# Kernel tuning notes

Hardware: AMD Instinct MI355X
Metric: run time of the kernel (lower is better)

The kernel has to match this reference:

```python
import jax, jax.numpy as jnp
import numpy as np

N_NODES = 50000
N_EDGES = 1600000
NFEAT, NHID, NCLASS = 256, 128, 40
DROPOUT_P = 0.5


def gcn_conv(x, W, b, src, dst, n):
    # PyG GCNConv: h = X W; add self-loops; symmetric norm D^-1/2 (A+I) D^-1/2.
    h = x @ W  # [N, out]
    loop = jnp.arange(n, dtype=src.dtype)
    s = jnp.concatenate([src, loop])  # [E+N]
    d = jnp.concatenate([dst, loop])
    deg = jax.ops.segment_sum(jnp.ones_like(d, dtype=h.dtype), d, num_segments=n)  # in-degree incl. self-loop
    dinv = jax.lax.rsqrt(jnp.maximum(deg, 1.0))
    norm = dinv[s] * dinv[d]  # [E+N]
    msg = h[s] * norm[:, None]  # [E+N, out] gather
    out = jax.ops.segment_sum(msg, d, num_segments=n)  # scatter-add
    return out + b


def setup_inputs() -> dict:
    key = jax.random.key(0)
    k = jax.random.split(key, 7)
    x = jax.random.normal(k[0], (N_NODES, NFEAT), dtype=jnp.float32)
    edge_index = jax.random.randint(k[1], (2, N_EDGES), 0, N_NODES, dtype=jnp.int64)
    W1 = jax.random.normal(k[2], (NFEAT, NHID), dtype=jnp.float32) * (1.0 / np.sqrt(NFEAT))
    b1 = jnp.zeros((NHID,), dtype=jnp.float32)
    W2 = jax.random.normal(k[3], (NHID, NCLASS), dtype=jnp.float32) * (1.0 / np.sqrt(NHID))
    b2 = jnp.zeros((NCLASS,), dtype=jnp.float32)
    keep = jax.random.bernoulli(k[4], 1.0 - DROPOUT_P, (N_NODES, NHID))
    drop_mask = keep.astype(jnp.float32) / (1.0 - DROPOUT_P)  # fixed training-mode dropout mask
    return {"x": x, "edge_index": edge_index, "W1": W1, "b1": b1, "W2": W2, "b2": b2, "drop_mask": drop_mask}


def reference(x, edge_index, W1, b1, W2, b2, drop_mask):
    src, dst = edge_index[0], edge_index[1]
    h = gcn_conv(x, W1, b1, src, dst, N_NODES)
    h = jax.nn.relu(h)
    h = h * drop_mask  # F.dropout(training=True) with fixed mask
    h = gcn_conv(h, W2, b2, src, dst, N_NODES)
    return jax.nn.log_softmax(h, axis=1)
```

## Files before the change

### kernel.cpp

```cpp
#include <hip/hip_runtime.h>
#include <hip/hip_fp16.h>
#include <math.h>

#define N_NODES 50000
#define N_EDGES 1600000
#define NFEAT 256
#define NHID 128
#define NCLASS 40

#define BSHIFT 7
#define NBUCK 391
#define CAP 5120
#define EPB 4096
#define SEGN 4
#define SEGSZ 12800

typedef _Float16 f16x8 __attribute__((ext_vector_type(8)));
typedef float f32x4 __attribute__((ext_vector_type(4)));

__global__ __launch_bounds__(256) void k_binA(const int* __restrict__ src,
                                              const int* __restrict__ dst,
                                              int* __restrict__ gcur,
                                              unsigned int* __restrict__ packed) {
    __shared__ int lhist[NBUCK];
    __shared__ int lbase[NBUCK];
    __shared__ int lcur[NBUCK];
    int t = threadIdx.x;
    for (int i = t; i < NBUCK; i += 256) { lhist[i] = 0; lcur[i] = 0; }
    __syncthreads();
    int e0 = blockIdx.x * EPB;
    int e1 = min(e0 + EPB, N_EDGES);
    for (int e = e0 + t; e < e1; e += 256) {
        int b = dst[e] >> BSHIFT;
        atomicAdd(&lhist[b], 1);
    }
    __syncthreads();
    for (int i = t; i < NBUCK; i += 256)
        lbase[i] = atomicAdd(&gcur[i], lhist[i]);
    __syncthreads();
    for (int e = e0 + t; e < e1; e += 256) {
        int d = dst[e];
        int b = d >> BSHIFT;
        int r = atomicAdd(&lcur[b], 1);
        int pos = lbase[b] + r;
        if (pos < CAP)
            packed[(size_t)b * CAP + pos] =
                ((unsigned int)src[e] << BSHIFT) | (unsigned int)(d & 127);
    }
}

__global__ __launch_bounds__(256) void k_binB(const int* __restrict__ gcur,
                                              const unsigned int* __restrict__ packed,
                                              unsigned short* __restrict__ esrc_seg,
                                              unsigned short* __restrict__ esrc_row,
                                              int* __restrict__ sbeg,
                                              int* __restrict__ scnt,
                                              int* __restrict__ row_beg,
                                              int* __restrict__ row_cnt,
                                              float* __restrict__ dinv) {
    __shared__ unsigned int sp[CAP];
    __shared__ int hist[512];
    __shared__ int scan[512];
    __shared__ int cur[512];
    __shared__ int psum[64];
    int b = blockIdx.x;
    int t = threadIdx.x;
    int cnt = min(gcur[b], CAP);
    for (int i = t; i < 512; i += 256) { hist[i] = 0; cur[i] = 0; }
    __syncthreads();
    const unsigned int* pin = packed + (size_t)b * CAP;
    for (int i = t; i < cnt; i += 256) {
        unsigned int w = pin[i];
        sp[i] = w;
        int srcv = (int)(w >> BSHIFT);
        atomicAdd(&hist[(srcv / SEGSZ) * 128 + (int)(w & 127u)], 1);
    }
    __syncthreads();
    if (t < 64) {
        int s = 0;
        #pragma unroll
        for (int j = 0; j < 8; j++) s += hist[t * 8 + j];
        psum[t] = s;
    }
    __syncthreads();
    if (t == 0) {
        int s = 0;
        for (int j = 0; j < 64; j++) { int v = psum[j]; psum[j] = s; s += v; }
    }
    __syncthreads();
    if (t < 64) {
        int s = psum[t];
        #pragma unroll
        for (int j = 0; j < 8; j++) { scan[t * 8 + j] = s; s += hist[t * 8 + j]; }
    }
    __syncthreads();
    for (int i = t; i < cnt; i += 256) {
        unsigned int w = sp[i];
        int srcv = (int)(w >> BSHIFT);
        int key = (srcv / SEGSZ) * 128 + (int)(w & 127u);
        int r = atomicAdd(&cur[key], 1);
        esrc_seg[(size_t)b * CAP + scan[key] + r] = (unsigned short)srcv;
    }
    if (t < 128) {
        int node = b * 128 + t;
        if (node < N_NODES) {
            int tot = 0;
            #pragma unroll
            for (int s = 0; s < SEGN; s++) {
                sbeg[node * 4 + s] = b * CAP + scan[s * 128 + t];
                scnt[node * 4 + s] = hist[s * 128 + t];
                tot += hist[s * 128 + t];
            }
            row_cnt[node] = tot;
            dinv[node] = rsqrtf((float)(tot + 1));
        }
    }
    __syncthreads();
    if (t < 128) { hist[t] = 0; cur[t] = 0; }
    __syncthreads();
    for (int i = t; i < cnt; i += 256) atomicAdd(&hist[sp[i] & 127u], 1);
    __syncthreads();
    if (t == 0) {
        int s = 0;
        for (int j = 0; j < 128; j++) { int v = hist[j]; scan[j] = s; s += v; }
    }
    __syncthreads();
    for (int i = t; i < cnt; i += 256) {
        unsigned int w = sp[i];
        int dl = (int)(w & 127u);
        int r = atomicAdd(&cur[dl], 1);
        esrc_row[(size_t)b * CAP + scan[dl] + r] = (unsigned short)(w >> BSHIFT);
    }
    if (t < 128) {
        int node = b * 128 + t;
        if (node < N_NODES) row_beg[node] = b * CAP + scan[t];
    }
}

__global__ __launch_bounds__(256) void k_prep(const float* __restrict__ W1,
                                              const float* __restrict__ W2,
                                              __half* __restrict__ w1t,
                                              __half* __restrict__ w2t,
                                              int* __restrict__ gcur) {
    int t = blockIdx.x * 256 + threadIdx.x;
    if (t < NBUCK) gcur[t] = 0;
    if (t < 128 * 256) {
        int n = t >> 8, k = t & 255;
        w1t[t] = __float2half(W1[k * NHID + n]);
    }
    if (t < 48 * 128) {
        int n = t >> 7, k = t & 127;
        w2t[t] = __float2half(n < NCLASS ? W2[k * NCLASS + n] : 0.0f);
    }
}

#define G1_LDA 72
#define G1_LDB 72
#define G1_LDE 136
__global__ __launch_bounds__(256) void k_gemm1(const float* __restrict__ x,
                                               const __half* __restrict__ w1t,
                                               __half* __restrict__ h1h) {
    __shared__ __half smem[64 * G1_LDA + 128 * G1_LDB];
    __half* sA = smem;
    __half* sB = smem + 64 * G1_LDA;
    int t = threadIdx.x;
    int rbase = blockIdx.x * 64;
    int lane = t & 63, wv = t >> 6;
    int m = lane & 15, quad = lane >> 4;
    f32x4 acc[8];
    #pragma unroll
    for (int i = 0; i < 8; i++) acc[i] = (f32x4)0.0f;

    int arow = t >> 2, aseg = t & 3;
    int grow = rbase + arow;
    bool avalid = grow < N_NODES;
    int bn = t >> 1, bseg = t & 1;

    for (int k0 = 0; k0 < NFEAT; k0 += 64) {
        const float4* gs = (const float4*)(x + (size_t)grow * NFEAT + k0 + aseg * 16);
        __half* ad = sA + arow * G1_LDA + aseg * 16;
        #pragma unroll
        for (int i = 0; i < 4; i++) {
            float4 v = avalid ? gs[i] : make_float4(0.f, 0.f, 0.f, 0.f);
            __half2 h0 = __float22half2_rn(make_float2(v.x, v.y));
            __half2 h1 = __float22half2_rn(make_float2(v.z, v.w));
            uint2 st;
            st.x = __builtin_bit_cast(unsigned int, h0);
            st.y = __builtin_bit_cast(unsigned int, h1);
            *(uint2*)(ad + i * 4) = st;
        }
        const uint4* ws4 = (const uint4*)(w1t + bn * NFEAT + k0 + bseg * 32);
        uint4* bd = (uint4*)(sB + bn * G1_LDB + bseg * 32);
        #pragma unroll
        for (int i = 0; i < 4; i++) bd[i] = ws4[i];
        __syncthreads();
        #pragma unroll
        for (int kk = 0; kk < 64; kk += 32) {
            f16x8 af = *(const f16x8*)(sA + (wv * 16 + m) * G1_LDA + kk + quad * 8);
            #pragma unroll
            for (int t8 = 0; t8 < 8; t8++) {
                f16x8 bf = *(const f16x8*)(sB + (t8 * 16 + m) * G1_LDB + kk + quad * 8);
                acc[t8] = __builtin_amdgcn_mfma_f32_16x16x32_f16(af, bf, acc[t8], 0, 0, 0);
            }
        }
        __syncthreads();
    }
    __half* eb = smem;
    #pragma unroll
    for (int t8 = 0; t8 < 8; t8++) {
        #pragma unroll
        for (int r = 0; r < 4; r++)
            eb[(wv * 16 + quad * 4 + r) * G1_LDE + t8 * 16 + m] = __float2half(acc[t8][r]);
    }
    __syncthreads();
    if (avalid) {
        const uint4* es = (const uint4*)(eb + arow * G1_LDE + aseg * 32);
        uint4* od = (uint4*)(h1h + (size_t)grow * NHID + aseg * 32);
        #pragma unroll
        for (int i = 0; i < 4; i++) od[i] = es[i];
    }
}

#define G2_LDA 136
#define G2_LDB 136
#define G2_LDE 72
__global__ __launch_bounds__(256) void k_gemm2(const __half* __restrict__ h1p,
                                               const __half* __restrict__ w2t,
                                               __half* __restrict__ h2p) {
    __shared__ __half smem[64 * G2_LDA + 48 * G2_LDB];
    __half* sA = smem;
    __half* sB = smem + 64 * G2_LDA;
    int t = threadIdx.x;
    int rbase = blockIdx.x * 64;
    int lane = t & 63, wv = t >> 6;
    int m = lane & 15, quad = lane >> 4;
    f32x4 acc[3];
    #pragma unroll
    for (int i = 0; i < 3; i++) acc[i] = (f32x4)0.0f;

    int arow = t >> 2, aseg = t & 3;
    int grow = rbase + arow;
    bool avalid = grow < N_NODES;

    #pragma unroll
    for (int i = 0; i < 3; i++) {
        int idx = t + i * 256;
        int n = idx >> 4, seg = idx & 15;
        *(uint4*)(sB + n * G2_LDB + seg * 8) = *(const uint4*)(w2t + n * NHID + seg * 8);
    }
    {
        const uint4* gs = (const uint4*)(h1p + (size_t)grow * NHID + aseg * 32);
        uint4* ad = (uint4*)(sA + arow * G2_LDA + aseg * 32);
        uint4 z; z.x = z.y = z.z = z.w = 0;
        #pragma unroll
        for (int i = 0; i < 4; i++) ad[i] = avalid ? gs[i] : z;
    }
    __syncthreads();
    #pragma unroll
    for (int kk = 0; kk < 128; kk += 32) {
        f16x8 af = *(const f16x8*)(sA + (wv * 16 + m) * G2_LDA + kk + quad * 8);
        #pragma unroll
        for (int t3 = 0; t3 < 3; t3++) {
            f16x8 bf = *(const f16x8*)(sB + (t3 * 16 + m) * G2_LDB + kk + quad * 8);
            acc[t3] = __builtin_amdgcn_mfma_f32_16x16x32_f16(af, bf, acc[t3], 0, 0, 0);
        }
    }
    __syncthreads();
    __half* eb = smem;
    #pragma unroll
    for (int t3 = 0; t3 < 3; t3++) {
        #pragma unroll
        for (int r = 0; r < 4; r++)
            eb[(wv * 16 + quad * 4 + r) * G2_LDE + t3 * 16 + m] = __float2half(acc[t3][r]);
    }
    {
        int zr = t >> 2, zc = 48 + (t & 3) * 4;
        uint2 z; z.x = z.y = 0;
        *(uint2*)(eb + zr * G2_LDE + zc) = z;
    }
    __syncthreads();
    #pragma unroll
    for (int i = 0; i < 2; i++) {
        int idx = t + i * 256;
        int row = idx >> 3, seg = idx & 7;
        int gr = rbase + row;
        if (gr < N_NODES)
            *(uint4*)(h2p + (size_t)gr * 64 + seg * 8) = *(const uint4*)(eb + row * G2_LDE + seg * 8);
    }
}

__device__ __forceinline__ void acc8f(float* acc, uint4 v, float d) {
    float2 a0 = __half22float2(__builtin_bit_cast(__half2, v.x));
    float2 a1 = __half22float2(__builtin_bit_cast(__half2, v.y));
    float2 a2 = __half22float2(__builtin_bit_cast(__half2, v.z));
    float2 a3 = __half22float2(__builtin_bit_cast(__half2, v.w));
    acc[0] = fmaf(a0.x, d, acc[0]); acc[1] = fmaf(a0.y, d, acc[1]);
    acc[2] = fmaf(a1.x, d, acc[2]); acc[3] = fmaf(a1.y, d, acc[3]);
    acc[4] = fmaf(a2.x, d, acc[4]); acc[5] = fmaf(a2.y, d, acc[5]);
    acc[6] = fmaf(a3.x, d, acc[6]); acc[7] = fmaf(a3.y, d, acc[7]);
}

__global__ __launch_bounds__(256) void k_agg1(const __half* __restrict__ h1h,
                                              const float* __restrict__ dinv,
                                              const int* __restrict__ sbeg,
                                              const int* __restrict__ scnt,
                                              const unsigned short* __restrict__ esrc_seg,
                                              const float* __restrict__ b1,
                                              const float* __restrict__ mask,
                                              __half* __restrict__ h1p) {
    int t = threadIdx.x;
    int qw = t >> 4, ln = t & 15;
    int nbase = blockIdx.x * 64;
    const uint4* hv4 = (const uint4*)h1h;
    __half2 hacc[4][4];
    __half2 hz = __half2half2(__float2half(0.0f));
    #pragma unroll
    for (int k = 0; k < 4; k++) {
        hacc[k][0] = hz; hacc[k][1] = hz; hacc[k][2] = hz; hacc[k][3] = hz;
    }
    for (int s = 0; s < SEGN; s++) {
        #pragma unroll
        for (int k = 0; k < 4; k++) {
            int node = nbase + qw * 4 + k;
            if (node >= N_NODES) continue;
            int beg = sbeg[node * 4 + s];
            int cn = scnt[node * 4 + s];
            for (int e0 = 0; e0 < cn; e0 += 16) {
                int idx = e0 + ln;
                int sv = (idx < cn) ? (int)esrc_seg[beg + idx] : 0;
                float dv = (idx < cn) ? dinv[sv] : 0.0f;
                int n4 = min(16, cn - e0);
                n4 = (n4 + 3) & ~3;
                for (int j = 0; j < n4; j += 4) {
                    int base = qw * 16 + j;
                    int sA = __shfl(sv, base + 0); float dA = __shfl(dv, base + 0);
                    int sB = __shfl(sv, base + 1); float dB = __shfl(dv, base + 1);
                    int sC = __shfl(sv, base + 2); float dC = __shfl(dv, base + 2);
                    int sD = __shfl(sv, base + 3); float dD = __shfl(dv, base + 3);
                    uint4 vA = hv4[(size_t)sA * 16 + ln];
                    uint4 vB = hv4[(size_t)sB * 16 + ln];
                    uint4 vC = hv4[(size_t)sC * 16 + ln];
                    uint4 vD = hv4[(size_t)sD * 16 + ln];
                    __half2 hA = __half2half2(__float2half(dA));
                    __half2 hB = __half2half2(__float2half(dB));
                    __half2 hC = __half2half2(__float2half(dC));
                    __half2 hD = __half2half2(__float2half(dD));
                    hacc[k][0] = __hfma2(__builtin_bit_cast(__half2, vA.x), hA, hacc[k][0]);
                    hacc[k][1] = __hfma2(__builtin_bit_cast(__half2, vA.y), hA, hacc[k][1]);
                    hacc[k][2] = __hfma2(__builtin_bit_cast(__half2, vA.z), hA, hacc[k][2]);
                    hacc[k][3] = __hfma2(__builtin_bit_cast(__half2, vA.w), hA, hacc[k][3]);
                    hacc[k][0] = __hfma2(__builtin_bit_cast(__half2, vB.x), hB, hacc[k][0]);
                    hacc[k][1] = __hfma2(__builtin_bit_cast(__half2, vB.y), hB, hacc[k][1]);
                    hacc[k][2] = __hfma2(__builtin_bit_cast(__half2, vB.z), hB, hacc[k][2]);
                    hacc[k][3] = __hfma2(__builtin_bit_cast(__half2, vB.w), hB, hacc[k][3]);
                    hacc[k][0] = __hfma2(__builtin_bit_cast(__half2, vC.x), hC, hacc[k][0]);
                    hacc[k][1] = __hfma2(__builtin_bit_cast(__half2, vC.y), hC, hacc[k][1]);
                    hacc[k][2] = __hfma2(__builtin_bit_cast(__half2, vC.z), hC, hacc[k][2]);
                    hacc[k][3] = __hfma2(__builtin_bit_cast(__half2, vC.w), hC, hacc[k][3]);
                    hacc[k][0] = __hfma2(__builtin_bit_cast(__half2, vD.x), hD, hacc[k][0]);
                    hacc[k][1] = __hfma2(__builtin_bit_cast(__half2, vD.y), hD, hacc[k][1]);
                    hacc[k][2] = __hfma2(__builtin_bit_cast(__half2, vD.z), hD, hacc[k][2]);
                    hacc[k][3] = __hfma2(__builtin_bit_cast(__half2, vD.w), hD, hacc[k][3]);
                }
            }
        }
    }
    #pragma unroll
    for (int k = 0; k < 4; k++) {
        int node = nbase + qw * 4 + k;
        if (node >= N_NODES) continue;
        float di = dinv[node];
        float acc[8];
        #pragma unroll
        for (int k2 = 0; k2 < 4; k2++) {
            float2 f = __half22float2(hacc[k][k2]);
            acc[2 * k2] = f.x; acc[2 * k2 + 1] = f.y;
        }
        uint4 sv4 = hv4[(size_t)node * 16 + ln];
        acc8f(acc, sv4, di);
        float4 bb0 = ((const float4*)b1)[ln * 2];
        float4 bb1 = ((const float4*)b1)[ln * 2 + 1];
        const float4* mrow = (const float4*)(mask + (size_t)node * NHID);
        float4 mm0 = mrow[ln * 2];
        float4 mm1 = mrow[ln * 2 + 1];
        float o0 = fmaxf(fmaf(acc[0], di, bb0.x), 0.f) * mm0.x;
        float o1 = fmaxf(fmaf(acc[1], di, bb0.y), 0.f) * mm0.y;
        float o2 = fmaxf(fmaf(acc[2], di, bb0.z), 0.f) * mm0.z;
        float o3 = fmaxf(fmaf(acc[3], di, bb0.w), 0.f) * mm0.w;
        float o4 = fmaxf(fmaf(acc[4], di, bb1.x), 0.f) * mm1.x;
        float o5 = fmaxf(fmaf(acc[5], di, bb1.y), 0.f) * mm1.y;
        float o6 = fmaxf(fmaf(acc[6], di, bb1.z), 0.f) * mm1.z;
        float o7 = fmaxf(fmaf(acc[7], di, bb1.w), 0.f) * mm1.w;
        __half2 p0 = __float22half2_rn(make_float2(o0, o1));
        __half2 p1 = __float22half2_rn(make_float2(o2, o3));
        __half2 p2 = __float22half2_rn(make_float2(o4, o5));
        __half2 p3 = __float22half2_rn(make_float2(o6, o7));
        uint4 st;
        st.x = __builtin_bit_cast(unsigned int, p0);
        st.y = __builtin_bit_cast(unsigned int, p1);
        st.z = __builtin_bit_cast(unsigned int, p2);
        st.w = __builtin_bit_cast(unsigned int, p3);
        ((uint4*)h1p)[(size_t)node * 16 + ln] = st;
    }
}

__global__ __launch_bounds__(64) void k_agg2(const __half* __restrict__ h2p,
                                             const float* __restrict__ dinv,
                                             const int* __restrict__ row_beg,
                                             const int* __restrict__ row_cnt,
                                             const unsigned short* __restrict__ esrc,
                                             const float* __restrict__ b2,
                                             float* __restrict__ out) {
    int i = blockIdx.x;
    int lane = threadIdx.x;
    int o8 = lane >> 3;
    int fl = lane & 7;
    const uint4* hv4 = (const uint4*)h2p;
    float di = dinv[i];
    __half2 hacc[4];
    __half2 hz = __half2half2(__float2half(0.0f));
    hacc[0] = hz; hacc[1] = hz; hacc[2] = hz; hacc[3] = hz;
    int s0 = row_beg[i], cnt = row_cnt[i];
    for (int base = 0; base < cnt; base += 64) {
        int idx = base + lane;
        int sv = (idx < cnt) ? (int)esrc[s0 + idx] : 0;
        float dv = (idx < cnt) ? dinv[sv] : 0.0f;
        int n = min(64, cnt - base);
        int nr = (n + 31) & ~31;
        for (int j = 0; j < nr; j += 32) {
            int ss[4]; __half2 dd[4]; uint4 vv[4];
            #pragma unroll
            for (int k = 0; k < 4; k++) {
                int jx = j + 8 * k + o8;
                ss[k] = __shfl(sv, jx);
                float df = __shfl(dv, jx);
                dd[k] = __half2half2(__float2half(df));
            }
            #pragma unroll
            for (int k = 0; k < 4; k++) vv[k] = hv4[(size_t)ss[k] * 8 + fl];
            #pragma unroll
            for (int k = 0; k < 4; k++) {
                hacc[0] = __hfma2(__builtin_bit_cast(__half2, vv[k].x), dd[k], hacc[0]);
                hacc[1] = __hfma2(__builtin_bit_cast(__half2, vv[k].y), dd[k], hacc[1]);
                hacc[2] = __hfma2(__builtin_bit_cast(__half2, vv[k].z), dd[k], hacc[2]);
                hacc[3] = __hfma2(__builtin_bit_cast(__half2, vv[k].w), dd[k], hacc[3]);
            }
        }
    }
    float acc[8];
    #pragma unroll
    for (int k2 = 0; k2 < 4; k2++) {
        float2 f = __half22float2(hacc[k2]);
        acc[2 * k2] = f.x; acc[2 * k2 + 1] = f.y;
    }
    if (o8 == 0) {
        uint4 sv4 = hv4[(size_t)i * 8 + fl];
        acc8f(acc, sv4, di);
    }
    #pragma unroll
    for (int k = 0; k < 8; k++) {
        acc[k] += __shfl_xor(acc[k], 8);
        acc[k] += __shfl_xor(acc[k], 16);
        acc[k] += __shfl_xor(acc[k], 32);
    }
    if (o8 == 0) {
        bool act = (fl < 5);
        float val[8];
        float m = -INFINITY;
        if (act) {
            float4 bb0 = ((const float4*)b2)[fl * 2];
            float4 bb1 = ((const float4*)b2)[fl * 2 + 1];
            val[0] = fmaf(acc[0], di, bb0.x);
            val[1] = fmaf(acc[1], di, bb0.y);
            val[2] = fmaf(acc[2], di, bb0.z);
            val[3] = fmaf(acc[3], di, bb0.w);
            val[4] = fmaf(acc[4], di, bb1.x);
            val[5] = fmaf(acc[5], di, bb1.y);
            val[6] = fmaf(acc[6], di, bb1.z);
            val[7] = fmaf(acc[7], di, bb1.w);
            #pragma unroll
            for (int k = 0; k < 8; k++) m = fmaxf(m, val[k]);
        }
        m = fmaxf(m, __shfl_xor(m, 1));
        m = fmaxf(m, __shfl_xor(m, 2));
        m = fmaxf(m, __shfl_xor(m, 4));
        float ss = 0.f;
        if (act) {
            #pragma unroll
            for (int k = 0; k < 8; k++) ss += expf(val[k] - m);
        }
        ss += __shfl_xor(ss, 1);
        ss += __shfl_xor(ss, 2);
        ss += __shfl_xor(ss, 4);
        if (act) {
            float ls = m + logf(ss);
            float4 r0 = make_float4(val[0] - ls, val[1] - ls, val[2] - ls, val[3] - ls);
            float4 r1 = make_float4(val[4] - ls, val[5] - ls, val[6] - ls, val[7] - ls);
            float4* orow = (float4*)(out + (size_t)i * NCLASS + fl * 8);
            orow[0] = r0;
            orow[1] = r1;
        }
    }
}

extern "C" void kernel_launch(void* const* d_in, const int* in_sizes, int n_in,
                              void* d_out, int out_size, void* d_ws, size_t ws_size,
                              hipStream_t stream) {
    const float* x    = (const float*)d_in[0];
    const int*   ei   = (const int*)d_in[1];
    const float* W1   = (const float*)d_in[2];
    const float* b1   = (const float*)d_in[3];
    const float* W2   = (const float*)d_in[4];
    const float* b2   = (const float*)d_in[5];
    const float* mask = (const float*)d_in[6];
    float* out = (float*)d_out;

    const int* src = ei;
    const int* dst = ei + N_EDGES;

    char* ws = (char*)d_ws;
    size_t off = 0;
    __half* h1p    = (__half*)(ws + off); off += (size_t)N_NODES * NHID * 2;
    __half* h1h    = (__half*)(ws + off); off += (size_t)N_NODES * NHID * 2;
    unsigned short* esrc_seg = (unsigned short*)(ws + off);
    off += ((size_t)NBUCK * CAP * 2 + 255) & ~(size_t)255;
    unsigned short* esrc_row = (unsigned short*)(ws + off);
    off += ((size_t)NBUCK * CAP * 2 + 255) & ~(size_t)255;
    int*   sbeg    = (int*)   (ws + off); off += (size_t)N_NODES * 4 * 4;
    int*   scnt    = (int*)   (ws + off); off += (size_t)N_NODES * 4 * 4;
    float* dinv    = (float*) (ws + off); off += 200192;
    int*   row_beg = (int*)   (ws + off); off += 200192;
    int*   row_cnt = (int*)   (ws + off); off += 200192;
    int*   gcur    = (int*)   (ws + off); off += 4096;
    __half* w1t    = (__half*)(ws + off); off += 128 * 256 * 2;
    __half* w2t    = (__half*)(ws + off); off += 48 * 128 * 2;

    unsigned int* packed = (unsigned int*)h1p;
    __half* h2p = h1h;

    k_prep<<<128, 256, 0, stream>>>(W1, W2, w1t, w2t, gcur);
    k_binA<<<(N_EDGES + EPB - 1) / EPB, 256, 0, stream>>>(src, dst, gcur, packed);
    k_binB<<<NBUCK, 256, 0, stream>>>(gcur, packed, esrc_seg, esrc_row,
                                      sbeg, scnt, row_beg, row_cnt, dinv);

    k_gemm1<<<(N_NODES + 63) / 64, 256, 0, stream>>>(x, w1t, h1h);
    k_agg1<<<(N_NODES + 63) / 64, 256, 0, stream>>>(h1h, dinv, sbeg, scnt,
                                                    esrc_seg, b1, mask, h1p);
    k_gemm2<<<(N_NODES + 63) / 64, 256, 0, stream>>>(h1p, w2t, h2p);
    k_agg2<<<N_NODES, 64, 0, stream>>>(h2p, dinv, row_beg, row_cnt, esrc_row, b2, out);
}
```

Measured before the change: 278.6 us.

## Fuse edge binning with first GEMM launch and batch agg1 gathers

Edge binning (binA) and the first feature GEMM are merged into one launch. Block indices below NG1 run the GEMM and the rest run binning, so the two independent stages overlap on the GPU and one kernel launch is saved. The shared-memory buffer is reused for the binning histograms. Separately, agg1 now handles 2 nodes per 16-lane group instead of 4, which doubles the grid, and it issues 8 neighbor-row gathers before accumulating to raise memory-level parallelism. The cost is more register pressure from the 8 in-flight uint4 loads, and the mixed-role blocks may be unevenly loaded.

After: 271.3 us. 1.03x faster.

```diff
diff --git a/kernel.cpp b/kernel.cpp
--- a/kernel.cpp
+++ b/kernel.cpp
@@ -14,38 +14,122 @@
 #define EPB 4096
 #define SEGN 4
 #define SEGSZ 12800
+#define NG1 782
 
 typedef _Float16 f16x8 __attribute__((ext_vector_type(8)));
 typedef float f32x4 __attribute__((ext_vector_type(4)));
 
-__global__ __launch_bounds__(256) void k_binA(const int* __restrict__ src,
-                                              const int* __restrict__ dst,
-                                              int* __restrict__ gcur,
-                                              unsigned int* __restrict__ packed) {
-    __shared__ int lhist[NBUCK];
-    __shared__ int lbase[NBUCK];
-    __shared__ int lcur[NBUCK];
+__global__ __launch_bounds__(256) void k_prep(const float* __restrict__ W1,
+                                              const float* __restrict__ W2,
+                                              __half* __restrict__ w1t,
+                                              __half* __restrict__ w2t,
+                                              int* __restrict__ gcur) {
+    int t = blockIdx.x * 256 + threadIdx.x;
+    if (t < NBUCK) gcur[t] = 0;
+    if (t < 128 * 256) {
+        int n = t >> 8, k = t & 255;
+        w1t[t] = __float2half(W1[k * NHID + n]);
+    }
+    if (t < 48 * 128) {
+        int n = t >> 7, k = t & 127;
+        w2t[t] = __float2half(n < NCLASS ? W2[k * NCLASS + n] : 0.0f);
+    }
+}
+
+#define G1_LDA 72
+#define G1_LDB 72
+#define G1_LDE 136
+__global__ __launch_bounds__(256) void k_binA_gemm1(
+        const int* __restrict__ src, const int* __restrict__ dst,
+        int* __restrict__ gcur, unsigned int* __restrict__ packed,
+        const float* __restrict__ x, const __half* __restrict__ w1t,
+        __half* __restrict__ h1h) {
+    __shared__ __half smem[64 * G1_LDA + 128 * G1_LDB];
     int t = threadIdx.x;
-    for (int i = t; i < NBUCK; i += 256) { lhist[i] = 0; lcur[i] = 0; }
-    __syncthreads();
-    int e0 = blockIdx.x * EPB;
-    int e1 = min(e0 + EPB, N_EDGES);
-    for (int e = e0 + t; e < e1; e += 256) {
-        int b = dst[e] >> BSHIFT;
-        atomicAdd(&lhist[b], 1);
-    }
-    __syncthreads();
-    for (int i = t; i < NBUCK; i += 256)
-        lbase[i] = atomicAdd(&gcur[i], lhist[i]);
-    __syncthreads();
-    for (int e = e0 + t; e < e1; e += 256) {
-        int d = dst[e];
-        int b = d >> BSHIFT;
-        int r = atomicAdd(&lcur[b], 1);
-        int pos = lbase[b] + r;
-        if (pos < CAP)
-            packed[(size_t)b * CAP + pos] =
-                ((unsigned int)src[e] << BSHIFT) | (unsigned int)(d & 127);
+    if (blockIdx.x >= NG1) {
+        int bid = blockIdx.x - NG1;
+        int* lhist = (int*)smem;
+        int* lbase = lhist + NBUCK;
+        int* lcur  = lbase + NBUCK;
+        for (int i = t; i < NBUCK; i += 256) { lhist[i] = 0; lcur[i] = 0; }
+        __syncthreads();
+        int e0 = bid * EPB;
+        int e1 = min(e0 + EPB, N_EDGES);
+        for (int e = e0 + t; e < e1; e += 256) {
+            int b = dst[e] >> BSHIFT;
+            atomicAdd(&lhist[b], 1);
+        }
+        __syncthreads();
+        for (int i = t; i < NBUCK; i += 256)
+            lbase[i] = atomicAdd(&gcur[i], lhist[i]);
+        __syncthreads();
+        for (int e = e0 + t; e < e1; e += 256) {
+            int d = dst[e];
+            int b = d >> BSHIFT;
+            int r = atomicAdd(&lcur[b], 1);
+            int pos = lbase[b] + r;
+            if (pos < CAP)
+                packed[(size_t)b * CAP + pos] =
+                    ((unsigned int)src[e] << BSHIFT) | (unsigned int)(d & 127);
+        }
+        return;
+    }
+    __half* sA = smem;
+    __half* sB = smem + 64 * G1_LDA;
+    int rbase = blockIdx.x * 64;
+    int lane = t & 63, wv = t >> 6;
+    int m = lane & 15, quad = lane >> 4;
+    f32x4 acc[8];
+    #pragma unroll
+    for (int i = 0; i < 8; i++) acc[i] = (f32x4)0.0f;
+
+    int arow = t >> 2, aseg = t & 3;
+    int grow = rbase + arow;
+    bool avalid = grow < N_NODES;
+    int bn = t >> 1, bseg = t & 1;
+
+    for (int k0 = 0; k0 < NFEAT; k0 += 64) {
+        const float4* gs = (const float4*)(x + (size_t)grow * NFEAT + k0 + aseg * 16);
+        __half* ad = sA + arow * G1_LDA + aseg * 16;
+        #pragma unroll
+        for (int i = 0; i < 4; i++) {
+            float4 v = avalid ? gs[i] : make_float4(0.f, 0.f, 0.f, 0.f);
+            __half2 h0 = __float22half2_rn(make_float2(v.x, v.y));
+            __half2 h1 = __float22half2_rn(make_float2(v.z, v.w));
+            uint2 st;
+            st.x = __builtin_bit_cast(unsigned int, h0);
+            st.y = __builtin_bit_cast(unsigned int, h1);
+            *(uint2*)(ad + i * 4) = st;
+        }
+        const uint4* ws4 = (const uint4*)(w1t + bn * NFEAT + k0 + bseg * 32);
+        uint4* bd = (uint4*)(sB + bn * G1_LDB + bseg * 32);
+        #pragma unroll
+        for (int i = 0; i < 4; i++) bd[i] = ws4[i];
+        __syncthreads();
+        #pragma unroll
+        for (int kk = 0; kk < 64; kk += 32) {
+            f16x8 af = *(const f16x8*)(sA + (wv * 16 + m) * G1_LDA + kk + quad * 8);
+            #pragma unroll
+            for (int t8 = 0; t8 < 8; t8++) {
+                f16x8 bf = *(const f16x8*)(sB + (t8 * 16 + m) * G1_LDB + kk + quad * 8);
+                acc[t8] = __builtin_amdgcn_mfma_f32_16x16x32_f16(af, bf, acc[t8], 0, 0, 0);
+            }
+        }
+        __syncthreads();
+    }
+    __half* eb = smem;
+    #pragma unroll
+    for (int t8 = 0; t8 < 8; t8++) {
+        #pragma unroll
+        for (int r = 0; r < 4; r++)
+            eb[(wv * 16 + quad * 4 + r) * G1_LDE + t8 * 16 + m] = __float2half(acc[t8][r]);
+    }
+    __syncthreads();
+    if (avalid) {
+        const uint4* es = (const uint4*)(eb + arow * G1_LDE + aseg * 32);
+        uint4* od = (uint4*)(h1h + (size_t)grow * NHID + aseg * 32);
+        #pragma unroll
+        for (int i = 0; i < 4; i++) od[i] = es[i];
     }
 }
 
@@ -137,90 +221,6 @@
     }
 }
 
-__global__ __launch_bounds__(256) void k_prep(const float* __restrict__ W1,
-                                              const float* __restrict__ W2,
-                                              __half* __restrict__ w1t,
-                                              __half* __restrict__ w2t,
-                                              int* __restrict__ gcur) {
-    int t = blockIdx.x * 256 + threadIdx.x;
-    if (t < NBUCK) gcur[t] = 0;
-    if (t < 128 * 256) {
-        int n = t >> 8, k = t & 255;
-        w1t[t] = __float2half(W1[k * NHID + n]);
-    }
-    if (t < 48 * 128) {
-        int n = t >> 7, k = t & 127;
-        w2t[t] = __float2half(n < NCLASS ? W2[k * NCLASS + n] : 0.0f);
-    }
-}
-
-#define G1_LDA 72
-#define G1_LDB 72
-#define G1_LDE 136
-__global__ __launch_bounds__(256) void k_gemm1(const float* __restrict__ x,
-                                               const __half* __restrict__ w1t,
-                                               __half* __restrict__ h1h) {
-    __shared__ __half smem[64 * G1_LDA + 128 * G1_LDB];
-    __half* sA = smem;
-    __half* sB = smem + 64 * G1_LDA;
-    int t = threadIdx.x;
-    int rbase = blockIdx.x * 64;
-    int lane = t & 63, wv = t >> 6;
-    int m = lane & 15, quad = lane >> 4;
-    f32x4 acc[8];
-    #pragma unroll
-    for (int i = 0; i < 8; i++) acc[i] = (f32x4)0.0f;
-
-    int arow = t >> 2, aseg = t & 3;
-    int grow = rbase + arow;
-    bool avalid = grow < N_NODES;
-    int bn = t >> 1, bseg = t & 1;
-
-    for (int k0 = 0; k0 < NFEAT; k0 += 64) {
-        const float4* gs = (const float4*)(x + (size_t)grow * NFEAT + k0 + aseg * 16);
-        __half* ad = sA + arow * G1_LDA + aseg * 16;
-        #pragma unroll
-        for (int i = 0; i < 4; i++) {
-            float4 v = avalid ? gs[i] : make_float4(0.f, 0.f, 0.f, 0.f);
-            __half2 h0 = __float22half2_rn(make_float2(v.x, v.y));
-            __half2 h1 = __float22half2_rn(make_float2(v.z, v.w));
-            uint2 st;
-            st.x = __builtin_bit_cast(unsigned int, h0);
-            st.y = __builtin_bit_cast(unsigned int, h1);
-            *(uint2*)(ad + i * 4) = st;
-        }
-        const uint4* ws4 = (const uint4*)(w1t + bn * NFEAT + k0 + bseg * 32);
-        uint4* bd = (uint4*)(sB + bn * G1_LDB + bseg * 32);
-        #pragma unroll
-        for (int i = 0; i < 4; i++) bd[i] = ws4[i];
-        __syncthreads();
-        #pragma unroll
-        for (int kk = 0; kk < 64; kk += 32) {
-            f16x8 af = *(const f16x8*)(sA + (wv * 16 + m) * G1_LDA + kk + quad * 8);
-            #pragma unroll
-            for (int t8 = 0; t8 < 8; t8++) {
-                f16x8 bf = *(const f16x8*)(sB + (t8 * 16 + m) * G1_LDB + kk + quad * 8);
-                acc[t8] = __builtin_amdgcn_mfma_f32_16x16x32_f16(af, bf, acc[t8], 0, 0, 0);
-            }
-        }
-        __syncthreads();
-    }
-    __half* eb = smem;
-    #pragma unroll
-    for (int t8 = 0; t8 < 8; t8++) {
-        #pragma unroll
-        for (int r = 0; r < 4; r++)
-            eb[(wv * 16 + quad * 4 + r) * G1_LDE + t8 * 16 + m] = __float2half(acc[t8][r]);
-    }
-    __syncthreads();
-    if (avalid) {
-        const uint4* es = (const uint4*)(eb + arow * G1_LDE + aseg * 32);
-        uint4* od = (uint4*)(h1h + (size_t)grow * NHID + aseg * 32);
-        #pragma unroll
-        for (int i = 0; i < 4; i++) od[i] = es[i];
-    }
-}
-
 #define G2_LDA 136
 #define G2_LDB 136
 #define G2_LDE 72
@@ -310,18 +310,18 @@
                                               __half* __restrict__ h1p) {
     int t = threadIdx.x;
     int qw = t >> 4, ln = t & 15;
-    int nbase = blockIdx.x * 64;
+    int nbase = blockIdx.x * 32;
     const uint4* hv4 = (const uint4*)h1h;
-    __half2 hacc[4][4];
+    __half2 hacc[2][4];
     __half2 hz = __half2half2(__float2half(0.0f));
     #pragma unroll
-    for (int k = 0; k < 4; k++) {
+    for (int k = 0; k < 2; k++) {
         hacc[k][0] = hz; hacc[k][1] = hz; hacc[k][2] = hz; hacc[k][3] = hz;
     }
     for (int s = 0; s < SEGN; s++) {
         #pragma unroll
-        for (int k = 0; k < 4; k++) {
-            int node = nbase + qw * 4 + k;
+        for (int k = 0; k < 2; k++) {
+            int node = nbase + qw * 2 + k;
             if (node >= N_NODES) continue;
             int beg = sbeg[node * 4 + s];
             int cn = scnt[node * 4 + s];
@@ -330,44 +330,31 @@
                 int sv = (idx < cn) ? (int)esrc_seg[beg + idx] : 0;
                 float dv = (idx < cn) ? dinv[sv] : 0.0f;
                 int n4 = min(16, cn - e0);
-                n4 = (n4 + 3) & ~3;
-                for (int j = 0; j < n4; j += 4) {
-                    int base = qw * 16 + j;
-                    int sA = __shfl(sv, base + 0); float dA = __shfl(dv, base + 0);
-                    int sB = __shfl(sv, base + 1); float dB = __shfl(dv, base + 1);
-                    int sC = __shfl(sv, base + 2); float dC = __shfl(dv, base + 2);
-                    int sD = __shfl(sv, base + 3); float dD = __shfl(dv, base + 3);
-                    uint4 vA = hv4[(size_t)sA * 16 + ln];
-                    uint4 vB = hv4[(size_t)sB * 16 + ln];
-                    uint4 vC = hv4[(size_t)sC * 16 + ln];
-                    uint4 vD = hv4[(size_t)sD * 16 + ln];
-                    __half2 hA = __half2half2(__float2half(dA));
-                    __half2 hB = __half2half2(__float2half(dB));
-                    __half2 hC = __half2half2(__float2half(dC));
-                    __half2 hD = __half2half2(__float2half(dD));
-                    hacc[k][0] = __hfma2(__builtin_bit_cast(__half2, vA.x), hA, hacc[k][0]);
-                    hacc[k][1] = __hfma2(__builtin_bit_cast(__half2, vA.y), hA, hacc[k][1]);
-                    hacc[k][2] = __hfma2(__builtin_bit_cast(__half2, vA.z), hA, hacc[k][2]);
-                    hacc[k][3] = __hfma2(__builtin_bit_cast(__half2, vA.w), hA, hacc[k][3]);
-                    hacc[k][0] = __hfma2(__builtin_bit_cast(__half2, vB.x), hB, hacc[k][0]);
-                    hacc[k][1] = __hfma2(__builtin_bit_cast(__half2, vB.y), hB, hacc[k][1]);
-                    hacc[k][2] = __hfma2(__builtin_bit_cast(__half2, vB.z), hB, hacc[k][2]);
-                    hacc[k][3] = __hfma2(__builtin_bit_cast(__half2, vB.w), hB, hacc[k][3]);
-                    hacc[k][0] = __hfma2(__builtin_bit_cast(__half2, vC.x), hC, hacc[k][0]);
-                    hacc[k][1] = __hfma2(__builtin_bit_cast(__half2, vC.y), hC, hacc[k][1]);
-                    hacc[k][2] = __hfma2(__builtin_bit_cast(__half2, vC.z), hC, hacc[k][2]);
-                    hacc[k][3] = __hfma2(__builtin_bit_cast(__half2, vC.w), hC, hacc[k][3]);
-                    hacc[k][0] = __hfma2(__builtin_bit_cast(__half2, vD.x), hD, hacc[k][0]);
-                    hacc[k][1] = __hfma2(__builtin_bit_cast(__half2, vD.y), hD, hacc[k][1]);
-                    hacc[k][2] = __hfma2(__builtin_bit_cast(__half2, vD.z), hD, hacc[k][2]);
-                    hacc[k][3] = __hfma2(__builtin_bit_cast(__half2, vD.w), hD, hacc[k][3]);
+                int n8 = (n4 + 7) & ~7;
+                for (int j = 0; j < n8; j += 8) {
+                    int ss[8]; float dd[8]; uint4 vv[8];
+                    #pragma unroll
+                    for (int u = 0; u < 8; u++) {
+                        ss[u] = __shfl(sv, qw * 16 + j + u);
+                        dd[u] = __shfl(dv, qw * 16 + j + u);
+                    }
+                    #pragma unroll
+                    for (int u = 0; u < 8; u++) vv[u] = hv4[(size_t)ss[u] * 16 + ln];
+                    #pragma unroll
+                    for (int u = 0; u < 8; u++) {
+                        __half2 h = __half2half2(__float2half(dd[u]));
+                        hacc[k][0] = __hfma2(__builtin_bit_cast(__half2, vv[u].x), h, hacc[k][0]);
+                        hacc[k][1] = __hfma2(__builtin_bit_cast(__half2, vv[u].y), h, hacc[k][1]);
+                        hacc[k][2] = __hfma2(__builtin_bit_cast(__half2, vv[u].z), h, hacc[k][2]);
+                        hacc[k][3] = __hfma2(__builtin_bit_cast(__half2, vv[u].w), h, hacc[k][3]);
+                    }
                 }
             }
         }
     }
     #pragma unroll
-    for (int k = 0; k < 4; k++) {
-        int node = nbase + qw * 4 + k;
+    for (int k = 0; k < 2; k++) {
+        int node = nbase + qw * 2 + k;
         if (node >= N_NODES) continue;
         float di = dinv[node];
         float acc[8];
@@ -539,12 +526,12 @@
     __half* h2p = h1h;
 
     k_prep<<<128, 256, 0, stream>>>(W1, W2, w1t, w2t, gcur);
-    k_binA<<<(N_EDGES + EPB - 1) / EPB, 256, 0, stream>>>(src, dst, gcur, packed);
+    k_binA_gemm1<<<NG1 + (N_EDGES + EPB - 1) / EPB, 256, 0, stream>>>(
+        src, dst, gcur, packed, x, w1t, h1h);
     k_binB<<<NBUCK, 256, 0, stream>>>(gcur, packed, esrc_seg, esrc_row,
                                       sbeg, scnt, row_beg, row_cnt, dinv);
 
-    k_gemm1<<<(N_NODES + 63) / 64, 256, 0, stream>>>(x, w1t, h1h);
-    k_agg1<<<(N_NODES + 63) / 64, 256, 0, stream>>>(h1h, dinv, sbeg, scnt,
+    k_agg1<<<(N_NODES + 31) / 32, 256, 0, stream>>>(h1h, dinv, sbeg, scnt,
                                                     esrc_seg, b1, mask, h1p);
     k_gemm2<<<(N_NODES + 63) / 64, 256, 0, stream>>>(h1p, w2t, h2p);
     k_agg2<<<N_NODES, 64, 0, stream>>>(h2p, dinv, row_beg, row_cnt, esrc_row, b2, out);
```
